# Optimization experiments

Measured on AMD Instinct MI355X. Metric: run time of the kernel, lower is better.

## Reference

```python
import jax, jax.numpy as jnp
import numpy as np

B, T, C, H = 4, 1024, 1024, 16
D = C // H  # head dim = 64


def setup_inputs() -> dict:
    key = jax.random.key(0)
    ks = jax.random.split(key, 12)
    s = 1.0 / np.sqrt(C)
    inp = {
        "x": jax.random.normal(ks[0], (B, T, C), jnp.float32),
        "Wq": jax.random.normal(ks[1], (C, C), jnp.float32) * s,
        "bq": jnp.zeros((C,), jnp.float32),
        "Wk": jax.random.normal(ks[2], (C, C), jnp.float32) * s,
        "bk": jnp.zeros((C,), jnp.float32),
        "Wv": jax.random.normal(ks[3], (C, C), jnp.float32) * s,
        "bv": jnp.zeros((C,), jnp.float32),
        "time_weighting": jnp.ones((H, T, T), jnp.float32),
        "head_mix_w": jax.random.normal(ks[4], (H, H), jnp.float32) * (1.0 / np.sqrt(H)),
        "Wp": jax.random.normal(ks[5], (C, C), jnp.float32) * s,
        "bp": jnp.zeros((C,), jnp.float32),
    }
    return inp


def reference(x, Wq, bq, Wk, bk, Wv, bv, time_weighting, head_mix_w, Wp, bp):
    Bx, Tx, Cx = x.shape
    half = Cx // 2
    # time_shift: first half of channels sees x shifted by one step (row 0 -> zeros)
    x_shift = jnp.pad(x, ((0, 0), (1, 0), (0, 0)))[:, :Tx, :half]
    xs = jnp.concatenate([x_shift, x[:, :, half:]], axis=-1)

    def heads(y):  # [B,T,C] -> [B,H,T,D]
        return y.reshape(Bx, Tx, H, D).transpose(0, 2, 1, 3)

    q = heads(xs @ Wq.T + bq)
    k = heads(xs @ Wk.T + bk)
    v = heads(xs @ Wv.T + bv)

    att = jnp.einsum("bhtd,bhsd->bhts", q, k) * (1.0 / np.sqrt(D))
    causal = jnp.tril(jnp.ones((Tx, Tx), bool))
    att = jnp.where(causal, att, -jnp.inf)
    att = jax.nn.softmax(att, axis=-1)
    att = att * time_weighting[:, :Tx, :Tx]
    # 1x1 conv across heads
    att = jnp.einsum("oh,bhts->bots", head_mix_w, att)

    y = jnp.einsum("bhts,bhsd->bhtd", att, v)
    y = y.transpose(0, 2, 1, 3).reshape(Bx, Tx, Cx)
    return y @ Wp.T + bp
```

## Files before the change

### kernel.cpp

```cpp
#include <hip/hip_runtime.h>
#include <hip/hip_bf16.h>

#define T_ 1024

typedef __attribute__((ext_vector_type(8))) short short8;
typedef __attribute__((ext_vector_type(4))) float f32x4;
typedef __bf16 bf16x8 __attribute__((ext_vector_type(8)));
typedef __attribute__((ext_vector_type(4))) unsigned short ushort4v;

__device__ __forceinline__ unsigned short f2bf(float f) {
    unsigned u = __float_as_uint(f);
    u += 0x7fffu + ((u >> 16) & 1u);
    return (unsigned short)(u >> 16);
}
__device__ __forceinline__ float bf2f(unsigned short s) {
    return __uint_as_float(((unsigned)s) << 16);
}
__device__ __forceinline__ unsigned short f2h(float f) {
    _Float16 h = (_Float16)f;
    return __builtin_bit_cast(unsigned short, h);
}
__device__ __forceinline__ float h2f(unsigned short u) {
    return (float)__builtin_bit_cast(_Float16, u);
}

__global__ __launch_bounds__(256) void k_convert(
    const float* __restrict__ s0, const float* __restrict__ s1,
    const float* __restrict__ s2, const float* __restrict__ s3,
    unsigned short* __restrict__ d0, unsigned short* __restrict__ d1,
    unsigned short* __restrict__ d2, unsigned short* __restrict__ d3) {
    const float* src; unsigned short* dst;
    switch (blockIdx.y) {
        case 0:  src = s0; dst = d0; break;
        case 1:  src = s1; dst = d1; break;
        case 2:  src = s2; dst = d2; break;
        default: src = s3; dst = d3; break;
    }
    int i = (blockIdx.x * 256 + threadIdx.x) * 4;
    float4 v = *(const float4*)(src + i);
    ushort4v ov = { f2bf(v.x), f2bf(v.y), f2bf(v.z), f2bf(v.w) };
    *(ushort4v*)(dst + i) = ov;
}

__global__ __launch_bounds__(256) void k_xs(const float* __restrict__ x,
                                            unsigned short* __restrict__ xs) {
    int idx = (blockIdx.x * 256 + threadIdx.x) * 4;
    int c = idx & 1023;
    int m = idx >> 10;
    int t = m & 1023;
    float4 v;
    if (c < 512) {
        if (t == 0) { v.x = v.y = v.z = v.w = 0.f; }
        else        { v = *(const float4*)(x + (size_t)(m - 1) * 1024 + c); }
    } else {
        v = *(const float4*)(x + (size_t)m * 1024 + c);
    }
    ushort4v ov = { f2bf(v.x), f2bf(v.y), f2bf(v.z), f2bf(v.w) };
    *(ushort4v*)(xs + (size_t)m * 1024 + c) = ov;
}

__device__ __forceinline__ void gemm_body(const unsigned short* __restrict__ A,
                                          const unsigned short* __restrict__ Bt,
                                          int m0, int n0, int tid, f32x4 acc[4][4],
                                          unsigned short (*As)[32], unsigned short (*Bs)[32]) {
    const int lane = tid & 63, w = tid >> 6;
    const int wr = w >> 1, wc = w & 1;
#pragma unroll
    for (int i = 0; i < 4; i++)
#pragma unroll
        for (int j = 0; j < 4; j++) acc[i][j] = (f32x4){0.f, 0.f, 0.f, 0.f};

    for (int k0 = 0; k0 < 1024; k0 += 32) {
        __syncthreads();
#pragma unroll
        for (int it = 0; it < 2; it++) {
            int ch = it * 256 + tid;
            int row = ch >> 2, c = ch & 3;
            int col = (c ^ ((row >> 1) & 3)) * 8;
            *(short8*)&As[row][col] = *(const short8*)(A + (size_t)(m0 + row) * 1024 + k0 + c * 8);
            *(short8*)&Bs[row][col] = *(const short8*)(Bt + (size_t)(n0 + row) * 1024 + k0 + c * 8);
        }
        __syncthreads();
        bf16x8 af[4], bg[4];
        int c = lane >> 4;
#pragma unroll
        for (int i = 0; i < 4; i++) {
            int row = wr * 64 + i * 16 + (lane & 15);
            af[i] = *(const bf16x8*)&As[row][(c ^ ((row >> 1) & 3)) * 8];
        }
#pragma unroll
        for (int j = 0; j < 4; j++) {
            int row = wc * 64 + j * 16 + (lane & 15);
            bg[j] = *(const bf16x8*)&Bs[row][(c ^ ((row >> 1) & 3)) * 8];
        }
#pragma unroll
        for (int i = 0; i < 4; i++)
#pragma unroll
            for (int j = 0; j < 4; j++)
                acc[i][j] = __builtin_amdgcn_mfma_f32_16x16x32_bf16(af[i], bg[j], acc[i][j], 0, 0, 0);
    }
}

__global__ __launch_bounds__(256) void k_gemm_qkv(
    const unsigned short* __restrict__ A,
    const unsigned short* __restrict__ wq, const unsigned short* __restrict__ wk,
    const unsigned short* __restrict__ wv,
    const float* __restrict__ bq, const float* __restrict__ bk, const float* __restrict__ bv,
    unsigned short* __restrict__ qo, unsigned short* __restrict__ ko,
    unsigned short* __restrict__ vo) {
    __shared__ unsigned short As[128][32];
    __shared__ unsigned short Bs[128][32];
    const int mat = blockIdx.y >> 3;
    const unsigned short* Bt = mat == 0 ? wq : (mat == 1 ? wk : wv);
    const float* bias = mat == 0 ? bq : (mat == 1 ? bk : bv);
    unsigned short* out = mat == 0 ? qo : (mat == 1 ? ko : vo);
    const int m0 = blockIdx.x * 128, n0 = (blockIdx.y & 7) * 128;
    const int tid = threadIdx.x, lane = tid & 63, w = tid >> 6;
    const int wr = w >> 1, wc = w & 1;
    f32x4 acc[4][4];
    gemm_body(A, Bt, m0, n0, tid, acc, As, Bs);
#pragma unroll
    for (int i = 0; i < 4; i++) {
        int mbase = m0 + wr * 64 + i * 16 + ((lane >> 4) << 2);
#pragma unroll
        for (int j = 0; j < 4; j++) {
            int n = n0 + wc * 64 + j * 16 + (lane & 15);
            float bv_ = bias[n];
            int h = n >> 6, d = n & 63;
#pragma unroll
            for (int r = 0; r < 4; r++) {
                int mm = mbase + r;
                int b = mm >> 10, t = mm & 1023;
                out[(size_t)((b * 16 + h) * 1024 + t) * 64 + d] = f2bf(acc[i][j][r] + bv_);
            }
        }
    }
}

__global__ __launch_bounds__(256) void k_gemm_out(
    const unsigned short* __restrict__ A, const unsigned short* __restrict__ Bt,
    const float* __restrict__ bias, float* __restrict__ out) {
    __shared__ unsigned short As[128][32];
    __shared__ unsigned short Bs[128][32];
    const int m0 = blockIdx.x * 128, n0 = blockIdx.y * 128;
    const int tid = threadIdx.x, lane = tid & 63, w = tid >> 6;
    const int wr = w >> 1, wc = w & 1;
    f32x4 acc[4][4];
    gemm_body(A, Bt, m0, n0, tid, acc, As, Bs);
#pragma unroll
    for (int i = 0; i < 4; i++) {
        int mbase = m0 + wr * 64 + i * 16 + ((lane >> 4) << 2);
#pragma unroll
        for (int j = 0; j < 4; j++) {
            int n = n0 + wc * 64 + j * 16 + (lane & 15);
            float bv_ = bias[n];
#pragma unroll
            for (int r = 0; r < 4; r++)
                out[(size_t)(mbase + r) * 1024 + n] = acc[i][j][r] + bv_;
        }
    }
}

__global__ __launch_bounds__(256) void k_scores(const unsigned short* __restrict__ qb,
                                                const unsigned short* __restrict__ kb,
                                                unsigned short* __restrict__ Sb,
                                                float* __restrict__ invb) {
    __shared__ unsigned short qs[64][64];
    __shared__ unsigned short ks[64][64];
    const int tid = threadIdx.x, lane = tid & 63, w = tid >> 6;
    const int t0 = (15 - (int)blockIdx.x) * 64;
    const int bh = blockIdx.y;
    const unsigned short* qp = qb + (size_t)bh * 65536;
    const unsigned short* kp = kb + (size_t)bh * 65536;

#pragma unroll
    for (int it = 0; it < 2; it++) {
        int ch = it * 256 + tid; int row = ch >> 3, c = ch & 7;
        *(short8*)&qs[row][(c ^ (row & 7)) * 8] = *(const short8*)(qp + (size_t)(t0 + row) * 64 + c * 8);
    }
    __syncthreads();
    const int row_a = w * 16 + (lane & 15);
    bf16x8 a0 = *(const bf16x8*)&qs[row_a][(((lane >> 4)    ) ^ (row_a & 7)) * 8];
    bf16x8 a1 = *(const bf16x8*)&qs[row_a][(((lane >> 4) + 4) ^ (row_a & 7)) * 8];
    const int tr = t0 + w * 16 + ((lane >> 4) << 2);
    float l_[4] = {0.f, 0.f, 0.f, 0.f};
    unsigned short* sp_out = Sb + (size_t)bh * ((size_t)T_ * T_);

    for (int s0 = 0; s0 <= t0 + 63; s0 += 64) {
        __syncthreads();
#pragma unroll
        for (int it = 0; it < 2; it++) {
            int ch = it * 256 + tid; int row = ch >> 3, c = ch & 7;
            *(short8*)&ks[row][(c ^ (row & 7)) * 8] = *(const short8*)(kp + (size_t)(s0 + row) * 64 + c * 8);
        }
        __syncthreads();
        f32x4 S[4];
#pragma unroll
        for (int sf = 0; sf < 4; sf++) {
            int row = sf * 16 + (lane & 15);
            bf16x8 b0 = *(const bf16x8*)&ks[row][(((lane >> 4)    ) ^ (row & 7)) * 8];
            bf16x8 b1 = *(const bf16x8*)&ks[row][(((lane >> 4) + 4) ^ (row & 7)) * 8];
            f32x4 z = (f32x4){0.f, 0.f, 0.f, 0.f};
            z = __builtin_amdgcn_mfma_f32_16x16x32_bf16(a0, b0, z, 0, 0, 0);
            z = __builtin_amdgcn_mfma_f32_16x16x32_bf16(a1, b1, z, 0, 0, 0);
            S[sf] = z;
        }
        float es[4][4];
#pragma unroll
        for (int sf = 0; sf < 4; sf++) {
            int s = s0 + sf * 16 + (lane & 15);
#pragma unroll
            for (int r = 0; r < 4; r++) {
                float sv = (s <= tr + r) ? S[sf][r] * 0.125f : -65504.f;
                es[sf][r] = __expf(sv);
                sp_out[(size_t)(tr + r) * T_ + s] = f2h(sv);
            }
        }
#pragma unroll
        for (int r = 0; r < 4; r++) {
            float ts = es[0][r] + es[1][r] + es[2][r] + es[3][r];
            ts += __shfl_xor(ts, 1);
            ts += __shfl_xor(ts, 2);
            ts += __shfl_xor(ts, 4);
            ts += __shfl_xor(ts, 8);
            l_[r] += ts;
        }
    }
    if ((lane & 15) == 0) {
#pragma unroll
        for (int r = 0; r < 4; r++) invb[(size_t)bh * T_ + tr + r] = 1.f / l_[r];
    }
}

__global__ __launch_bounds__(256) void k_mixnorm(unsigned short* __restrict__ Sb,
                                                 const float* __restrict__ invb,
                                                 const float* __restrict__ tw,
                                                 const float* __restrict__ mixw) {
    const int t = blockIdx.y, b = blockIdx.z;
    if ((int)(blockIdx.x * 256) > (t | 63)) return;
    const int s = blockIdx.x * 256 + threadIdx.x;
    __shared__ float mw[256];
    __shared__ float inv_s[16];
    mw[threadIdx.x] = mixw[threadIdx.x];
    if (threadIdx.x < 16) inv_s[threadIdx.x] = invb[(size_t)(b * 16 + threadIdx.x) * T_ + t];
    __syncthreads();
    float p[16];
    size_t base = (size_t)b * 16 * 1048576 + (size_t)t * 1024 + s;
    size_t twoff = (size_t)t * 1024 + s;
#pragma unroll
    for (int h = 0; h < 16; h++)
        p[h] = __expf(h2f(Sb[base + (size_t)h * 1048576])) * inv_s[h] * tw[(size_t)h * 1048576 + twoff];
#pragma unroll
    for (int o = 0; o < 16; o++) {
        float acc = 0.f;
#pragma unroll
        for (int h = 0; h < 16; h++) acc += mw[o * 16 + h] * p[h];
        Sb[base + (size_t)o * 1048576] = f2bf(acc);
    }
}

__global__ __launch_bounds__(256) void k_av(const unsigned short* __restrict__ att,
                                            const unsigned short* __restrict__ vb,
                                            unsigned short* __restrict__ y1) {
    __shared__ unsigned short as_[64][64];
    __shared__ unsigned short vs[64][72];
    const int tid = threadIdx.x, lane = tid & 63, w = tid >> 6;
    const int t0 = (15 - (int)blockIdx.x) * 64;
    const int bh = blockIdx.y;
    const int b = bh >> 4, h = bh & 15;
    const unsigned short* ap = att + (size_t)bh * 1048576;
    const unsigned short* vp = vb + (size_t)bh * 65536;
    f32x4 acc[4];
#pragma unroll
    for (int j = 0; j < 4; j++) acc[j] = (f32x4){0.f, 0.f, 0.f, 0.f};

    for (int s0 = 0; s0 <= t0 + 63; s0 += 64) {
        __syncthreads();
#pragma unroll
        for (int it = 0; it < 2; it++) {
            int ch = it * 256 + tid;
            int row = ch >> 3, c = ch & 7;
            *(short8*)&as_[row][(c ^ (row & 7)) * 8] =
                *(const short8*)(ap + (size_t)(t0 + row) * 1024 + s0 + c * 8);
            int sp = ch >> 3, dc = (ch & 7) * 8;
            short8 vv = *(const short8*)(vp + (size_t)(s0 + sp) * 64 + dc);
#pragma unroll
            for (int i = 0; i < 8; i++) vs[dc + i][sp] = ((unsigned short*)&vv)[i];
        }
        __syncthreads();
        const int row_a = w * 16 + (lane & 15);
#pragma unroll
        for (int ks = 0; ks < 2; ks++) {
            bf16x8 af = *(const bf16x8*)&as_[row_a][((((lane >> 4) + 4 * ks)) ^ (row_a & 7)) * 8];
#pragma unroll
            for (int j = 0; j < 4; j++) {
                bf16x8 bg = *(const bf16x8*)&vs[j * 16 + (lane & 15)][ks * 32 + (lane >> 4) * 8];
                acc[j] = __builtin_amdgcn_mfma_f32_16x16x32_bf16(af, bg, acc[j], 0, 0, 0);
            }
        }
    }

    int t = t0 + w * 16 + ((lane >> 4) << 2);
#pragma unroll
    for (int j = 0; j < 4; j++) {
        int d = j * 16 + (lane & 15);
#pragma unroll
        for (int r = 0; r < 4; r++)
            y1[(size_t)(b * 1024 + t + r) * 1024 + h * 64 + d] = f2bf(acc[j][r]);
    }
}

extern "C" void kernel_launch(void* const* d_in, const int* in_sizes, int n_in,
                              void* d_out, int out_size, void* d_ws, size_t ws_size,
                              hipStream_t stream) {
    (void)in_sizes; (void)n_in; (void)out_size; (void)ws_size;
    const float* x    = (const float*)d_in[0];
    const float* Wq   = (const float*)d_in[1];
    const float* bq   = (const float*)d_in[2];
    const float* Wk   = (const float*)d_in[3];
    const float* bk   = (const float*)d_in[4];
    const float* Wv   = (const float*)d_in[5];
    const float* bv   = (const float*)d_in[6];
    const float* tw   = (const float*)d_in[7];
    const float* mixw = (const float*)d_in[8];
    const float* Wp   = (const float*)d_in[9];
    const float* bp   = (const float*)d_in[10];

    char* ws = (char*)d_ws;
    size_t off = 0;
    auto alloc = [&](size_t bytes) -> char* {
        char* p = ws + off;
        off += (bytes + 255) & ~(size_t)255;
        return p;
    };
    unsigned short* xs  = (unsigned short*)alloc((size_t)4096 * 1024 * 2);
    unsigned short* wqb = (unsigned short*)alloc((size_t)1024 * 1024 * 2);
    unsigned short* wkb = (unsigned short*)alloc((size_t)1024 * 1024 * 2);
    unsigned short* wvb = (unsigned short*)alloc((size_t)1024 * 1024 * 2);
    unsigned short* wpb = (unsigned short*)alloc((size_t)1024 * 1024 * 2);
    unsigned short* qb  = (unsigned short*)alloc((size_t)64 * 1024 * 64 * 2);
    unsigned short* kb  = (unsigned short*)alloc((size_t)64 * 1024 * 64 * 2);
    unsigned short* vb_ = (unsigned short*)alloc((size_t)64 * 1024 * 64 * 2);
    unsigned short* Sb  = (unsigned short*)alloc((size_t)64 * 1024 * 1024 * 2);
    float*          invb = (float*)alloc((size_t)64 * 1024 * 4);
    unsigned short* y1  = (unsigned short*)alloc((size_t)4096 * 1024 * 2);

    k_convert<<<dim3(1024, 4), 256, 0, stream>>>(Wq, Wk, Wv, Wp, wqb, wkb, wvb, wpb);
    k_xs<<<4096, 256, 0, stream>>>(x, xs);
    k_gemm_qkv<<<dim3(32, 24), 256, 0, stream>>>(xs, wqb, wkb, wvb, bq, bk, bv, qb, kb, vb_);
    k_scores<<<dim3(16, 64), 256, 0, stream>>>(qb, kb, Sb, invb);
    k_mixnorm<<<dim3(4, 1024, 4), 256, 0, stream>>>(Sb, invb, tw, mixw);
    k_av<<<dim3(16, 64), 256, 0, stream>>>(Sb, vb_, y1);
    k_gemm_out<<<dim3(32, 8), 256, 0, stream>>>(y1, wpb, bp, (float*)d_out);
}
```

Measured before the change: 355.7 us.

## Store exp scores in fp16 and do head mixing with MFMA

The scores kernel now writes exp(score) as fp16 instead of the raw scaled logit, and accumulates the row sums per lane, doing the cross-lane shuffle reduction once after the loop instead of every tile. The mixing kernel therefore skips its exponential. It replaces the scalar 16x16 head-mix loop with an fp16 MFMA over an LDS-staged tile of probabilities. Masked positions become exact zeros. The risks are fp16 overflow of exp for large scores and lower-precision mixing weights and probabilities.

Result: slower. 368.8 us (+3.7%).

```diff
diff --git a/kernel.cpp b/kernel.cpp
--- a/kernel.cpp
+++ b/kernel.cpp
@@ -6,6 +6,7 @@
 typedef __attribute__((ext_vector_type(8))) short short8;
 typedef __attribute__((ext_vector_type(4))) float f32x4;
 typedef __bf16 bf16x8 __attribute__((ext_vector_type(8)));
+typedef _Float16 f16x8 __attribute__((ext_vector_type(8)));
 typedef __attribute__((ext_vector_type(4))) unsigned short ushort4v;
 
 __device__ __forceinline__ unsigned short f2bf(float f) {
@@ -163,7 +164,7 @@
 
 __global__ __launch_bounds__(256) void k_scores(const unsigned short* __restrict__ qb,
                                                 const unsigned short* __restrict__ kb,
-                                                unsigned short* __restrict__ Sb,
+                                                unsigned short* __restrict__ Eb,
                                                 float* __restrict__ invb) {
     __shared__ unsigned short qs[64][64];
     __shared__ unsigned short ks[64][64];
@@ -184,7 +185,7 @@
     bf16x8 a1 = *(const bf16x8*)&qs[row_a][(((lane >> 4) + 4) ^ (row_a & 7)) * 8];
     const int tr = t0 + w * 16 + ((lane >> 4) << 2);
     float l_[4] = {0.f, 0.f, 0.f, 0.f};
-    unsigned short* sp_out = Sb + (size_t)bh * ((size_t)T_ * T_);
+    unsigned short* ep = Eb + (size_t)bh * ((size_t)T_ * T_);
 
     for (int s0 = 0; s0 <= t0 + 63; s0 += 64) {
         __syncthreads();
@@ -205,26 +206,25 @@
             z = __builtin_amdgcn_mfma_f32_16x16x32_bf16(a1, b1, z, 0, 0, 0);
             S[sf] = z;
         }
-        float es[4][4];
 #pragma unroll
         for (int sf = 0; sf < 4; sf++) {
             int s = s0 + sf * 16 + (lane & 15);
 #pragma unroll
             for (int r = 0; r < 4; r++) {
-                float sv = (s <= tr + r) ? S[sf][r] * 0.125f : -65504.f;
-                es[sf][r] = __expf(sv);
-                sp_out[(size_t)(tr + r) * T_ + s] = f2h(sv);
+                float es = (s <= tr + r) ? __expf(S[sf][r] * 0.125f) : 0.f;
+                l_[r] += es;
+                ep[(size_t)(tr + r) * T_ + s] = f2h(es);
             }
         }
-#pragma unroll
-        for (int r = 0; r < 4; r++) {
-            float ts = es[0][r] + es[1][r] + es[2][r] + es[3][r];
-            ts += __shfl_xor(ts, 1);
-            ts += __shfl_xor(ts, 2);
-            ts += __shfl_xor(ts, 4);
-            ts += __shfl_xor(ts, 8);
-            l_[r] += ts;
-        }
+    }
+#pragma unroll
+    for (int r = 0; r < 4; r++) {
+        float ts = l_[r];
+        ts += __shfl_xor(ts, 1);
+        ts += __shfl_xor(ts, 2);
+        ts += __shfl_xor(ts, 4);
+        ts += __shfl_xor(ts, 8);
+        l_[r] = ts;
     }
     if ((lane & 15) == 0) {
 #pragma unroll
@@ -232,30 +232,68 @@
     }
 }
 
-__global__ __launch_bounds__(256) void k_mixnorm(unsigned short* __restrict__ Sb,
-                                                 const float* __restrict__ invb,
-                                                 const float* __restrict__ tw,
-                                                 const float* __restrict__ mixw) {
+__global__ __launch_bounds__(256) void k_mix2(unsigned short* __restrict__ Sb,
+                                              const float* __restrict__ invb,
+                                              const float* __restrict__ tw,
+                                              const float* __restrict__ mixw) {
     const int t = blockIdx.y, b = blockIdx.z;
-    if ((int)(blockIdx.x * 256) > (t | 63)) return;
-    const int s = blockIdx.x * 256 + threadIdx.x;
-    __shared__ float mw[256];
+    const int send = t | 63;
+    if ((int)(blockIdx.x * 256) > send) return;
+    const int tid = threadIdx.x, lane = tid & 63, w = tid >> 6;
+    const int s = blockIdx.x * 256 + tid;
+    __shared__ unsigned short p2[256][32];
     __shared__ float inv_s[16];
-    mw[threadIdx.x] = mixw[threadIdx.x];
-    if (threadIdx.x < 16) inv_s[threadIdx.x] = invb[(size_t)(b * 16 + threadIdx.x) * T_ + t];
+    if (tid < 16) inv_s[tid] = invb[(size_t)(b * 16 + tid) * T_ + t];
     __syncthreads();
-    float p[16];
-    size_t base = (size_t)b * 16 * 1048576 + (size_t)t * 1024 + s;
-    size_t twoff = (size_t)t * 1024 + s;
-#pragma unroll
-    for (int h = 0; h < 16; h++)
-        p[h] = __expf(h2f(Sb[base + (size_t)h * 1048576])) * inv_s[h] * tw[(size_t)h * 1048576 + twoff];
-#pragma unroll
-    for (int o = 0; o < 16; o++) {
-        float acc = 0.f;
-#pragma unroll
-        for (int h = 0; h < 16; h++) acc += mw[o * 16 + h] * p[h];
-        Sb[base + (size_t)o * 1048576] = f2bf(acc);
+
+    const bool live = (s <= send);
+    unsigned rowbase = (unsigned)t * 1024u + (unsigned)s;
+    unsigned short* plane0 = Sb + (size_t)b * 16 * 1048576;
+    short8 lo, hi;
+#pragma unroll
+    for (int hh = 0; hh < 8; hh++) {
+        float e0 = 0.f, e1 = 0.f;
+        if (live) {
+            e0 = h2f(plane0[(size_t)hh * 1048576 + rowbase]) * inv_s[hh]
+                 * tw[(size_t)hh * 1048576 + rowbase];
+            e1 = h2f(plane0[(size_t)(hh + 8) * 1048576 + rowbase]) * inv_s[hh + 8]
+                 * tw[(size_t)(hh + 8) * 1048576 + rowbase];
+        }
+        ((unsigned short*)&lo)[hh] = f2h(e0);
+        ((unsigned short*)&hi)[hh] = f2h(e1);
+    }
+    short8 zz = {0, 0, 0, 0, 0, 0, 0, 0};
+    int sw = (tid >> 1) & 3;
+    *(short8*)&p2[tid][(0 ^ sw) * 8] = lo;
+    *(short8*)&p2[tid][(1 ^ sw) * 8] = hi;
+    *(short8*)&p2[tid][(2 ^ sw) * 8] = zz;
+    *(short8*)&p2[tid][(3 ^ sw) * 8] = zz;
+
+    short8 afb;
+#pragma unroll
+    for (int j = 0; j < 8; j++) {
+        int k = (lane >> 4) * 8 + j;
+        float mv = (k < 16) ? mixw[(lane & 15) * 16 + k] : 0.f;
+        ((unsigned short*)&afb)[j] = f2h(mv);
+    }
+    f16x8 af = __builtin_bit_cast(f16x8, afb);
+    __syncthreads();
+
+#pragma unroll
+    for (int g = 0; g < 4; g++) {
+        int pos = (w * 4 + g) * 16 + (lane & 15);
+        f16x8 bf = *(const f16x8*)&p2[pos][(((lane >> 4)) ^ ((pos >> 1) & 3)) * 8];
+        f32x4 d = (f32x4){0.f, 0.f, 0.f, 0.f};
+        d = __builtin_amdgcn_mfma_f32_16x16x32_f16(af, bf, d, 0, 0, 0);
+        int spos = blockIdx.x * 256 + pos;
+        if (spos <= send) {
+            unsigned ob = (unsigned)t * 1024u + (unsigned)spos;
+#pragma unroll
+            for (int r = 0; r < 4; r++) {
+                int o = (lane >> 4) * 4 + r;
+                plane0[(size_t)o * 1048576 + ob] = f2bf(d[r]);
+            }
+        }
     }
 }
 
@@ -349,7 +387,7 @@
     k_xs<<<4096, 256, 0, stream>>>(x, xs);
     k_gemm_qkv<<<dim3(32, 24), 256, 0, stream>>>(xs, wqb, wkb, wvb, bq, bk, bv, qb, kb, vb_);
     k_scores<<<dim3(16, 64), 256, 0, stream>>>(qb, kb, Sb, invb);
-    k_mixnorm<<<dim3(4, 1024, 4), 256, 0, stream>>>(Sb, invb, tw, mixw);
+    k_mix2<<<dim3(4, 1024, 4), 256, 0, stream>>>(Sb, invb, tw, mixw);
     k_av<<<dim3(16, 64), 256, 0, stream>>>(Sb, vb_, y1);
     k_gemm_out<<<dim3(32, 8), 256, 0, stream>>>(y1, wpb, bp, (float*)d_out);
 }
```
